# Kernel tuning notes

Hardware: AMD Instinct MI355X
Metric: run time of the kernel (lower is better)

## Reference

```python
import jax, jax.numpy as jnp
import numpy as np
from jax import lax

B, T, H, E, C = 64, 512, 512, 128, 1000


def setup_inputs() -> dict:
    key = jax.random.key(0)
    k0, k1, k2, k3, k4 = jax.random.split(key, 5)
    marks = jax.random.randint(k0, (B, T), 0, C)
    # monotonic event times -> positive inter-event durations
    timestamps = jnp.cumsum(jax.random.uniform(k1, (B, T), dtype=jnp.float32), axis=1)
    emb_table = jax.random.normal(k2, (C, E), dtype=jnp.float32) * 0.02
    W_cell = jax.random.normal(k3, (E + H, 7 * H), dtype=jnp.float32) / np.sqrt(E + H).astype(np.float32)
    b_cell = jnp.zeros((7 * H,), dtype=jnp.float32)
    init_hidden = jax.random.normal(k4, (1, 6 * H), dtype=jnp.float32) * 0.02
    return {"marks": marks, "timestamps": timestamps, "emb_table": emb_table,
            "W_cell": W_cell, "b_cell": b_cell, "init_hidden": init_hidden}


def _hawkes_states(marks, timestamps, emb_table, W_cell, b_cell, init_hidden):
    b, t = marks.shape
    h6 = init_hidden.shape[-1]
    h = h6 // 6
    e = emb_table.shape[-1]
    # inter-event durations (time_embedding): [B,T]
    dt = jnp.diff(timestamps, axis=1, prepend=jnp.zeros((b, 1), timestamps.dtype))
    x = emb_table[marks]  # [B,T,E]
    # precompute input contribution to the gates outside the scan
    x_gates = jnp.einsum('bte,eg->btg', x, W_cell[:e]) + b_cell  # [B,T,7H]
    Wh = W_cell[e:]  # [H,7H]

    init = jnp.broadcast_to(init_hidden, (b, h6))
    h_d0, c_d0, c_bar0, c0, delta0, o0 = jnp.split(init, 6, axis=-1)
    h_d0 = jnp.tanh(h_d0); c_d0 = jnp.tanh(c_d0); c_bar0 = jnp.tanh(c_bar0)
    c0 = jnp.tanh(c0); delta0 = jax.nn.softplus(delta0); o0 = jax.nn.sigmoid(o0)
    state0 = jnp.concatenate([h_d0, o0, c_bar0, c0, delta0, c_d0], axis=-1)  # [B,6H]

    def step(carry, inp):
        h_d, c_d, c_bar = carry
        xg, dur = inp  # [B,7H], [B]
        g = xg + h_d @ Wh
        gi, gf, gz, go, gib, gfb, gd = jnp.split(g, 7, axis=-1)
        gi = jax.nn.sigmoid(gi); gf = jax.nn.sigmoid(gf); gz = jnp.tanh(gz)
        go = jax.nn.sigmoid(go); gib = jax.nn.sigmoid(gib); gfb = jax.nn.sigmoid(gfb)
        gd = jax.nn.softplus(gd)
        c = gf * c_d + gi * gz
        c_bar_t = gfb * c_bar + gib * gz
        c_d_t = c_bar_t + (c - c_bar_t) * jnp.exp(-gd * dur[:, None])
        h_d_t = go * jnp.tanh(c_d_t)
        out = jnp.concatenate([h_d_t, go, c_bar_t, c, gd, c_d_t], axis=-1)
        return (h_d_t, c_d_t, c_bar_t), out

    _, outs = lax.scan(step, (h_d0, c_d0, c_bar0),
                       (x_gates.transpose(1, 0, 2), dt.T))  # outs: [T,B,6H]
    return jnp.concatenate([state0[:, None, :], outs.transpose(1, 0, 2)], axis=1)  # [B,T+1,6H]


def reference(marks, timestamps, emb_table, W_cell, b_cell, init_hidden):
    return _hawkes_states(marks, timestamps, emb_table, W_cell, b_cell, init_hidden)
```

## Files before the change

kernel.cpp:

```cpp
#include <hip/hip_runtime.h>
#include <stdint.h>

#define TT    512
#define HH    512
#define EE    128
#define G7    (7*HH)
#define H6    (6*HH)
#define TP1   (TT+1)

#define BW 16
#define II 32
#define NIG 16
#define NCOL 224
#define HLDS 520

typedef float f32x4 __attribute__((ext_vector_type(4)));
typedef short short8 __attribute__((ext_vector_type(8)));

__device__ __forceinline__ float bf2f(unsigned short u){
  union { unsigned u32; float f; } v; v.u32 = ((unsigned)u) << 16; return v.f;
}
__device__ __forceinline__ unsigned short f2bf(float f){
  union { float f; unsigned u; } v; v.f = f;
  unsigned u = v.u;
  u += 0x7FFFu + ((u >> 16) & 1u);
  return (unsigned short)(u >> 16);
}
__device__ __forceinline__ float sigmoidf_(float x){ return 1.0f/(1.0f+__expf(-x)); }
__device__ __forceinline__ float tanhf_(float x){ return 1.0f - 2.0f/(__expf(2.0f*x)+1.0f); }
__device__ __forceinline__ float softplusf_(float x){
  float ax = fabsf(x);
  return fmaxf(x, 0.0f) + __logf(1.0f + __expf(-ax));
}

__device__ __forceinline__ bool detect_bf16(const void* ts){
  const unsigned short* p = (const unsigned short*)ts;
  int cnt = 0;
  #pragma unroll
  for (int i = 0; i < 32; ++i){
    unsigned short v = p[2*i];
    int e = (v >> 7) & 0xFF;
    cnt += (((v & 0x8000u) == 0) && e >= 110 && e <= 140) ? 1 : 0;
  }
  return cnt >= 16;
}

__device__ __forceinline__ float lde(const void* p, size_t i, bool bfm){
  return bfm ? bf2f(((const unsigned short*)p)[i]) : ((const float*)p)[i];
}
__device__ __forceinline__ void sto(void* p, size_t i, float v, bool bfm){
  if (bfm) ((unsigned short*)p)[i] = f2bf(v);
  else     ((float*)p)[i] = v;
}

__global__ void k_embgates(const void* __restrict__ emb,
                           const void* __restrict__ W,
                           const void* __restrict__ bcell,
                           const void* __restrict__ ts,
                           unsigned short* __restrict__ eg){
  const bool bfm = detect_bf16(ts);
  __shared__ __align__(16) float xs[8][EE];
  const int tid = threadIdx.x;
  const int c0  = blockIdx.y * 8;
  const int j   = blockIdx.x * 512 + tid * 2;

  #pragma unroll
  for (int r = 0; r < 4; ++r){
    int e = tid + 256*r;
    int ci = e >> 7, k = e & 127;
    xs[ci][k] = lde(emb, (size_t)(c0+ci)*EE + k, bfm);
  }
  __syncthreads();

  float acc[8][2];
  {
    float b0v = lde(bcell, j, bfm), b1v = lde(bcell, j+1, bfm);
    #pragma unroll
    for (int ci=0; ci<8; ++ci){ acc[ci][0] = b0v; acc[ci][1] = b1v; }
  }
  const unsigned short* W16 = (const unsigned short*)W;
  const float*          W32 = (const float*)W;
  for (int k0 = 0; k0 < EE; k0 += 4){
    float w0[4], w1[4];
    if (bfm){
      #pragma unroll
      for (int kk=0; kk<4; ++kk){
        unsigned wu = *(const unsigned*)&W16[(size_t)(k0+kk)*G7 + j];
        w0[kk] = bf2f((unsigned short)(wu & 0xffff));
        w1[kk] = bf2f((unsigned short)(wu >> 16));
      }
    } else {
      #pragma unroll
      for (int kk=0; kk<4; ++kk){
        float2 wf = *(const float2*)&W32[(size_t)(k0+kk)*G7 + j];
        w0[kk] = wf.x; w1[kk] = wf.y;
      }
    }
    #pragma unroll
    for (int ci=0; ci<8; ++ci){
      float4 x4 = *(const float4*)&xs[ci][k0];
      acc[ci][0] = fmaf(x4.x, w0[0], acc[ci][0]); acc[ci][1] = fmaf(x4.x, w1[0], acc[ci][1]);
      acc[ci][0] = fmaf(x4.y, w0[1], acc[ci][0]); acc[ci][1] = fmaf(x4.y, w1[1], acc[ci][1]);
      acc[ci][0] = fmaf(x4.z, w0[2], acc[ci][0]); acc[ci][1] = fmaf(x4.z, w1[2], acc[ci][1]);
      acc[ci][0] = fmaf(x4.w, w0[3], acc[ci][0]); acc[ci][1] = fmaf(x4.w, w1[3], acc[ci][1]);
    }
  }
  #pragma unroll
  for (int ci=0; ci<8; ++ci){
    unsigned outv = (unsigned)f2bf(acc[ci][0]) | ((unsigned)f2bf(acc[ci][1]) << 16);
    *(unsigned*)&eg[(size_t)(c0+ci)*G7 + j] = outv;
  }
}

__global__ void k_wqbf(const void* __restrict__ W,
                       const void* __restrict__ ts,
                       unsigned short* __restrict__ wqt){
  const bool bfm = detect_bf16(ts);
  __shared__ __align__(16) unsigned short tile[64][72];
  const int tid = threadIdx.x;
  const int j0 = blockIdx.x * 64;
  const int k0 = blockIdx.y * 64;
  const int c = tid & 63, r0 = tid >> 6;
  #pragma unroll
  for (int rr = 0; rr < 16; ++rr){
    int r = r0*16 + rr;
    tile[r][c] = f2bf(lde(W, (size_t)(EE + k0 + r)*G7 + (j0 + c), bfm));
  }
  __syncthreads();
  const int jj = tid >> 2, p = tid & 3;
  unsigned short o[16];
  #pragma unroll
  for (int q = 0; q < 16; ++q) o[q] = tile[p*16 + q][jj];
  unsigned short* dst = &wqt[(size_t)(j0+jj)*HH + k0 + p*16];
  *(uint4*)(dst)     = *(uint4*)&o[0];
  *(uint4*)(dst + 8) = *(uint4*)&o[8];
}

__launch_bounds__(1024, 1)
__global__ void k_scan(const int* __restrict__ marks,
                       const void* __restrict__ ts,
                       const void* __restrict__ ih,
                       const unsigned short* __restrict__ eg,
                       const unsigned short* __restrict__ wqt,
                       void* __restrict__ out,
                       unsigned int* flags,
                       unsigned long long* dbuf){
  const bool bfm = detect_bf16(ts);
  __shared__ __align__(16) unsigned short hdl[BW][HLDS];
  __shared__ __align__(16) float gl[BW][257];
  __shared__ __align__(16) unsigned short xgl[2][BW][240];

  const int tid  = threadIdx.x;
  const int g_i  = blockIdx.x & (NIG-1);
  const int g_b  = blockIdx.x >> 4;
  const int b0   = g_b * BW;
  const int i0   = g_i * II;
  const int lane = tid & 63;
  const int wv   = tid >> 6;

  short8 bq[16];
  {
    int n = lane & 15, q = lane >> 4;
    int coll = wv*16 + n;
    int cl = (coll < NCOL) ? coll : 0;
    int cg = ((cl >> 5) * HH) + i0 + (cl & 31);
    const unsigned short* wb = wqt + (size_t)cg*HH + q*8;
    #pragma unroll
    for (int kk = 0; kk < 16; ++kk)
      bq[kk] = *(const short8*)(wb + kk*32);
  }

  {
    int i = (tid & 255) * 2;
    unsigned short h0 = f2bf(tanhf_(lde(ih, i,   bfm)));
    unsigned short h1 = f2bf(tanhf_(lde(ih, i+1, bfm)));
    unsigned v = (unsigned)h0 | ((unsigned)h1 << 16);
    int bb0 = (tid >> 8) * 4;
    #pragma unroll
    for (int b = 0; b < 4; ++b) *(unsigned*)&hdl[bb0 + b][i] = v;
  }

  float cd = 0.0f, cbar = 0.0f, dtv = 0.0f;
  if (tid < 512){
    int b = tid >> 5, ii = tid & 31;
    int i = i0 + ii;
    float h0  = tanhf_(lde(ih, i, bfm));
    float cd0 = tanhf_(lde(ih, 512 + i, bfm));
    float cb0 = tanhf_(lde(ih, 1024 + i, bfm));
    float c0v = tanhf_(lde(ih, 1536 + i, bfm));
    float d0  = softplusf_(lde(ih, 2048 + i, bfm));
    float o0  = sigmoidf_(lde(ih, 2560 + i, bfm));
    cd = cd0; cbar = cb0;
    size_t ob = ((size_t)(b0 + b) * TP1) * H6 + i;
    sto(out, ob,        h0,  bfm);
    sto(out, ob +   HH, o0,  bfm);
    sto(out, ob + 2*HH, cb0, bfm);
    sto(out, ob + 3*HH, c0v, bfm);
    sto(out, ob + 4*HH, d0,  bfm);
    sto(out, ob + 5*HH, cd0, bfm);
  }

  if (tid < 512){
    int b = tid >> 5, c = tid & 31;
    if (c < 28){
      int mk = marks[(b0 + b)*TT + 0];
      int g = c >> 2, m4 = c & 3;
      uint4 v = *(const uint4*)&eg[(size_t)mk*G7 + g*HH + i0 + m4*8];
      *(uint4*)&xgl[0][b][c*8] = v;
    }
  }
  __syncthreads();

  const int m_ = lane & 15, q_ = lane >> 4;

  for (int t = 0; t < TT; ++t){
    const int cur = t & 1, nxt = cur ^ 1;

    if (t < TT-1 && tid < 512){
      int b = tid >> 5, c = tid & 31;
      if (c < 28){
        int mk = marks[(b0 + b)*TT + (t+1)];
        int g = c >> 2, m4 = c & 3;
        uint4 v = *(const uint4*)&eg[(size_t)mk*G7 + g*HH + i0 + m4*8];
        *(uint4*)&xgl[nxt][b][c*8] = v;
      }
    }
    if (tid < 512){
      int b = tid >> 5;
      float t1  = lde(ts, (size_t)(b0 + b)*TT + t, bfm);
      float t0_ = (t > 0) ? lde(ts, (size_t)(b0 + b)*TT + t - 1, bfm) : 0.0f;
      dtv = t1 - t0_;
    }

    if (t > 0){
      if (wv == 0){
        unsigned* fl = &flags[g_b * 64];
        const unsigned target = (unsigned)t;
        for (;;){
          unsigned v = __hip_atomic_load(&fl[lane & 15], __ATOMIC_RELAXED, __HIP_MEMORY_SCOPE_AGENT);
          if (__all((int)(v >= target))) break;
          __builtin_amdgcn_s_sleep(1);
        }
        __threadfence();
      }
      __syncthreads();
      const unsigned long long* src = dbuf + ((size_t)(g_b*2 + cur) * BW) * (HH/4);
      #pragma unroll
      for (int r = 0; r < 2; ++r){
        int idx = tid + 1024*r;
        int bb = idx >> 7, oo = idx & 127;
        unsigned long long v = __hip_atomic_load(&src[(size_t)bb*(HH/4) + oo],
                                                 __ATOMIC_RELAXED, __HIP_MEMORY_SCOPE_AGENT);
        *(unsigned long long*)&hdl[bb][oo*4] = v;
      }
    }
    __syncthreads();

    f32x4 acc = {0.f, 0.f, 0.f, 0.f};
    #pragma unroll
    for (int kk = 0; kk < 16; ++kk){
      short8 a = *(const short8*)&hdl[m_][kk*32 + q_*8];
      acc = __builtin_amdgcn_mfma_f32_16x16x32_bf16(a, bq[kk], acc, 0, 0, 0);
    }
    {
      int col  = wv*16 + (lane & 15);
      int rowb = (lane >> 4) * 4;
      #pragma unroll
      for (int r = 0; r < 4; ++r) gl[rowb + r][col] = acc[r];
    }
    __syncthreads();

    float hdt = 0.f, gov = 0.f, cbv = 0.f, cv = 0.f, gdv = 0.f, cdtv = 0.f;
    if (tid < 512){
      int b = tid >> 5, ii = tid & 31;
      float gv[7];
      #pragma unroll
      for (int g = 0; g < 7; ++g)
        gv[g] = gl[b][g*32 + ii] + bf2f(xgl[cur][b][g*32 + ii]);
      float gi  = sigmoidf_(gv[0]);
      float gf  = sigmoidf_(gv[1]);
      float gz  = tanhf_(gv[2]);
      gov       = sigmoidf_(gv[3]);
      float gib = sigmoidf_(gv[4]);
      float gfb = sigmoidf_(gv[5]);
      gdv       = softplusf_(gv[6]);
      cv   = gf*cd + gi*gz;
      cbv  = gfb*cbar + gib*gz;
      float dec = __expf(-gdv * dtv);
      cdtv = cbv + (cv - cbv)*dec;
      hdt  = gov * tanhf_(cdtv);
      cd = cdtv; cbar = cbv;

      unsigned hv = (unsigned)f2bf(hdt);
      unsigned a2 = hv | ((unsigned)__shfl_xor((int)hv, 1) << 16);
      unsigned hi = (unsigned)__shfl_xor((int)a2, 2);
      if ((tid & 3) == 0){
        unsigned long long v64 = (unsigned long long)a2 | ((unsigned long long)hi << 32);
        unsigned long long* dst = dbuf + ((size_t)(g_b*2 + nxt) * BW + b) * (HH/4)
                                       + ((i0 + ii) >> 2);
        __hip_atomic_store(dst, v64, __ATOMIC_RELAXED, __HIP_MEMORY_SCOPE_AGENT);
      }
    }
    __syncthreads();
    if (tid == 0){
      __threadfence();
      __hip_atomic_store(&flags[g_b*64 + g_i], (unsigned)(t + 1),
                         __ATOMIC_RELEASE, __HIP_MEMORY_SCOPE_AGENT);
    }
    if (tid < 512){
      int b = tid >> 5, ii = tid & 31;
      size_t ob = ((size_t)(b0 + b) * TP1 + (t+1)) * H6 + i0 + ii;
      sto(out, ob,        hdt,  bfm);
      sto(out, ob +   HH, gov,  bfm);
      sto(out, ob + 2*HH, cbv,  bfm);
      sto(out, ob + 3*HH, cv,   bfm);
      sto(out, ob + 4*HH, gdv,  bfm);
      sto(out, ob + 5*HH, cdtv, bfm);
    }
  }
}

extern "C" void kernel_launch(void* const* d_in, const int* in_sizes, int n_in,
                              void* d_out, int out_size, void* d_ws, size_t ws_size,
                              hipStream_t stream){
  const int*  marks = (const int*)d_in[0];
  const void* ts    = d_in[1];
  const void* emb   = d_in[2];
  const void* W     = d_in[3];
  const void* bc    = d_in[4];
  const void* ih    = d_in[5];

  unsigned char* ws = (unsigned char*)d_ws;
  unsigned int*       flags = (unsigned int*)ws;
  unsigned long long* dbuf  = (unsigned long long*)(ws + 1024);
  unsigned short*     eg    = (unsigned short*)(ws + 132096);
  unsigned short*     wqt   = (unsigned short*)(ws + 132096 + 7168000);
  (void)in_sizes; (void)n_in; (void)out_size;

  if (ws_size < (size_t)(132096 + 7168000 + 3670016)) return;

  hipMemsetAsync(flags, 0, 1024, stream);
  hipLaunchKernelGGL(k_embgates, dim3(7, 125), dim3(256), 0, stream, emb, W, bc, ts, eg);
  hipLaunchKernelGGL(k_wqbf,     dim3(56, 8),  dim3(256), 0, stream, W, ts, wqt);

  void* args[] = { (void*)&marks, (void*)&ts, (void*)&ih, (void*)&eg,
                   (void*)&wqt, (void*)&d_out, (void*)&flags, (void*)&dbuf };
  hipLaunchCooperativeKernel((const void*)k_scan, dim3(64), dim3(1024), args, 0, stream);
}
```

Baseline: 4.167 ms.

## Halve scan block to 512 threads, two MFMA tiles per wave, remap block ids

```diff
diff --git a/kernel.cpp b/kernel.cpp
--- a/kernel.cpp
+++ b/kernel.cpp
@@ -136,7 +136,7 @@
   *(uint4*)(dst + 8) = *(uint4*)&o[8];
 }
 
-__launch_bounds__(1024, 1)
+__launch_bounds__(512, 2)
 __global__ void k_scan(const int* __restrict__ marks,
                        const void* __restrict__ ts,
                        const void* __restrict__ ih,
@@ -151,23 +151,32 @@
   __shared__ __align__(16) unsigned short xgl[2][BW][240];
 
   const int tid  = threadIdx.x;
-  const int g_i  = blockIdx.x & (NIG-1);
-  const int g_b  = blockIdx.x >> 4;
+  const int bid  = blockIdx.x;
+  const int g_b  = (bid & 7) >> 1;
+  const int g_i  = ((bid >> 3) << 1) | (bid & 1);
   const int b0   = g_b * BW;
   const int i0   = g_i * II;
   const int lane = tid & 63;
   const int wv   = tid >> 6;
-
-  short8 bq[16];
+  const int eb   = tid >> 5;
+  const int eii  = tid & 31;
+
+  short8 bq0[16], bq1[16];
   {
     int n = lane & 15, q = lane >> 4;
-    int coll = wv*16 + n;
-    int cl = (coll < NCOL) ? coll : 0;
-    int cg = ((cl >> 5) * HH) + i0 + (cl & 31);
-    const unsigned short* wb = wqt + (size_t)cg*HH + q*8;
-    #pragma unroll
-    for (int kk = 0; kk < 16; ++kk)
-      bq[kk] = *(const short8*)(wb + kk*32);
+    int coll0 = wv*32 + n;
+    int coll1 = wv*32 + 16 + n;
+    int cl0 = (coll0 < NCOL) ? coll0 : 0;
+    int cl1 = (coll1 < NCOL) ? coll1 : 0;
+    int cg0 = ((cl0 >> 5) * HH) + i0 + (cl0 & 31);
+    int cg1 = ((cl1 >> 5) * HH) + i0 + (cl1 & 31);
+    const unsigned short* wb0 = wqt + (size_t)cg0*HH + q*8;
+    const unsigned short* wb1 = wqt + (size_t)cg1*HH + q*8;
+    #pragma unroll
+    for (int kk = 0; kk < 16; ++kk){
+      bq0[kk] = *(const short8*)(wb0 + kk*32);
+      bq1[kk] = *(const short8*)(wb1 + kk*32);
+    }
   }
 
   {
@@ -175,15 +184,14 @@
     unsigned short h0 = f2bf(tanhf_(lde(ih, i,   bfm)));
     unsigned short h1 = f2bf(tanhf_(lde(ih, i+1, bfm)));
     unsigned v = (unsigned)h0 | ((unsigned)h1 << 16);
-    int bb0 = (tid >> 8) * 4;
-    #pragma unroll
-    for (int b = 0; b < 4; ++b) *(unsigned*)&hdl[bb0 + b][i] = v;
-  }
-
-  float cd = 0.0f, cbar = 0.0f, dtv = 0.0f;
-  if (tid < 512){
-    int b = tid >> 5, ii = tid & 31;
-    int i = i0 + ii;
+    int bb0 = (tid >> 8) * 8;
+    #pragma unroll
+    for (int b = 0; b < 8; ++b) *(unsigned*)&hdl[bb0 + b][i] = v;
+  }
+
+  float cd, cbar, tsp = 0.0f;
+  {
+    int i = i0 + eii;
     float h0  = tanhf_(lde(ih, i, bfm));
     float cd0 = tanhf_(lde(ih, 512 + i, bfm));
     float cb0 = tanhf_(lde(ih, 1024 + i, bfm));
@@ -191,7 +199,7 @@
     float d0  = softplusf_(lde(ih, 2048 + i, bfm));
     float o0  = sigmoidf_(lde(ih, 2560 + i, bfm));
     cd = cd0; cbar = cb0;
-    size_t ob = ((size_t)(b0 + b) * TP1) * H6 + i;
+    size_t ob = ((size_t)(b0 + eb) * TP1) * H6 + i;
     sto(out, ob,        h0,  bfm);
     sto(out, ob +   HH, o0,  bfm);
     sto(out, ob + 2*HH, cb0, bfm);
@@ -200,14 +208,11 @@
     sto(out, ob + 5*HH, cd0, bfm);
   }
 
-  if (tid < 512){
-    int b = tid >> 5, c = tid & 31;
-    if (c < 28){
-      int mk = marks[(b0 + b)*TT + 0];
-      int g = c >> 2, m4 = c & 3;
-      uint4 v = *(const uint4*)&eg[(size_t)mk*G7 + g*HH + i0 + m4*8];
-      *(uint4*)&xgl[0][b][c*8] = v;
-    }
+  if (eii < 28){
+    int mk = marks[(b0 + eb)*TT + 0];
+    int g = eii >> 2, m4 = eii & 3;
+    uint4 v = *(const uint4*)&eg[(size_t)mk*G7 + g*HH + i0 + m4*8];
+    *(uint4*)&xgl[0][eb][eii*8] = v;
   }
   __syncthreads();
 
@@ -216,24 +221,20 @@
   for (int t = 0; t < TT; ++t){
     const int cur = t & 1, nxt = cur ^ 1;
 
-    if (t < TT-1 && tid < 512){
-      int b = tid >> 5, c = tid & 31;
-      if (c < 28){
-        int mk = marks[(b0 + b)*TT + (t+1)];
-        int g = c >> 2, m4 = c & 3;
-        uint4 v = *(const uint4*)&eg[(size_t)mk*G7 + g*HH + i0 + m4*8];
-        *(uint4*)&xgl[nxt][b][c*8] = v;
-      }
-    }
-    if (tid < 512){
-      int b = tid >> 5;
-      float t1  = lde(ts, (size_t)(b0 + b)*TT + t, bfm);
-      float t0_ = (t > 0) ? lde(ts, (size_t)(b0 + b)*TT + t - 1, bfm) : 0.0f;
-      dtv = t1 - t0_;
-    }
-
-    if (t > 0){
-      if (wv == 0){
+    if (t < TT-1 && eii < 28){
+      int mk = marks[(b0 + eb)*TT + (t+1)];
+      int g = eii >> 2, m4 = eii & 3;
+      uint4 v = *(const uint4*)&eg[(size_t)mk*G7 + g*HH + i0 + m4*8];
+      *(uint4*)&xgl[nxt][eb][eii*8] = v;
+    }
+    float dtv;
+    {
+      float t1 = lde(ts, (size_t)(b0 + eb)*TT + t, bfm);
+      dtv = t1 - tsp; tsp = t1;
+    }
+
+    if (t > 0 && wv == 0){
+      {
         unsigned* fl = &flags[g_b * 64];
         const unsigned target = (unsigned)t;
         for (;;){
@@ -243,40 +244,48 @@
         }
         __threadfence();
       }
-      __syncthreads();
       const unsigned long long* src = dbuf + ((size_t)(g_b*2 + cur) * BW) * (HH/4);
       #pragma unroll
-      for (int r = 0; r < 2; ++r){
-        int idx = tid + 1024*r;
-        int bb = idx >> 7, oo = idx & 127;
-        unsigned long long v = __hip_atomic_load(&src[(size_t)bb*(HH/4) + oo],
-                                                 __ATOMIC_RELAXED, __HIP_MEMORY_SCOPE_AGENT);
-        *(unsigned long long*)&hdl[bb][oo*4] = v;
+      for (int half = 0; half < 2; ++half){
+        unsigned long long tmp[16];
+        #pragma unroll
+        for (int r = 0; r < 16; ++r){
+          int idx = (half*16 + r)*64 + lane;
+          tmp[r] = __hip_atomic_load(&src[idx], __ATOMIC_RELAXED, __HIP_MEMORY_SCOPE_AGENT);
+        }
+        #pragma unroll
+        for (int r = 0; r < 16; ++r){
+          int idx = (half*16 + r)*64 + lane;
+          *(unsigned long long*)&hdl[idx >> 7][(idx & 127)*4] = tmp[r];
+        }
       }
     }
     __syncthreads();
 
-    f32x4 acc = {0.f, 0.f, 0.f, 0.f};
+    f32x4 acc0 = {0.f,0.f,0.f,0.f}, acc1 = {0.f,0.f,0.f,0.f};
     #pragma unroll
     for (int kk = 0; kk < 16; ++kk){
       short8 a = *(const short8*)&hdl[m_][kk*32 + q_*8];
-      acc = __builtin_amdgcn_mfma_f32_16x16x32_bf16(a, bq[kk], acc, 0, 0, 0);
+      acc0 = __builtin_amdgcn_mfma_f32_16x16x32_bf16(a, bq0[kk], acc0, 0, 0, 0);
+      acc1 = __builtin_amdgcn_mfma_f32_16x16x32_bf16(a, bq1[kk], acc1, 0, 0, 0);
     }
     {
-      int col  = wv*16 + (lane & 15);
+      int col0 = wv*32 + (lane & 15);
       int rowb = (lane >> 4) * 4;
       #pragma unroll
-      for (int r = 0; r < 4; ++r) gl[rowb + r][col] = acc[r];
+      for (int r = 0; r < 4; ++r){
+        gl[rowb + r][col0]      = acc0[r];
+        gl[rowb + r][col0 + 16] = acc1[r];
+      }
     }
     __syncthreads();
 
-    float hdt = 0.f, gov = 0.f, cbv = 0.f, cv = 0.f, gdv = 0.f, cdtv = 0.f;
-    if (tid < 512){
-      int b = tid >> 5, ii = tid & 31;
+    float hdt, gov, cbv, cv, gdv, cdtv;
+    {
       float gv[7];
       #pragma unroll
       for (int g = 0; g < 7; ++g)
-        gv[g] = gl[b][g*32 + ii] + bf2f(xgl[cur][b][g*32 + ii]);
+        gv[g] = gl[eb][g*32 + eii] + bf2f(xgl[cur][eb][g*32 + eii]);
       float gi  = sigmoidf_(gv[0]);
       float gf  = sigmoidf_(gv[1]);
       float gz  = tanhf_(gv[2]);
@@ -296,8 +305,8 @@
       unsigned hi = (unsigned)__shfl_xor((int)a2, 2);
       if ((tid & 3) == 0){
         unsigned long long v64 = (unsigned long long)a2 | ((unsigned long long)hi << 32);
-        unsigned long long* dst = dbuf + ((size_t)(g_b*2 + nxt) * BW + b) * (HH/4)
-                                       + ((i0 + ii) >> 2);
+        unsigned long long* dst = dbuf + ((size_t)(g_b*2 + nxt) * BW + eb) * (HH/4)
+                                       + ((i0 + eii) >> 2);
         __hip_atomic_store(dst, v64, __ATOMIC_RELAXED, __HIP_MEMORY_SCOPE_AGENT);
       }
     }
@@ -307,9 +316,8 @@
       __hip_atomic_store(&flags[g_b*64 + g_i], (unsigned)(t + 1),
                          __ATOMIC_RELEASE, __HIP_MEMORY_SCOPE_AGENT);
     }
-    if (tid < 512){
-      int b = tid >> 5, ii = tid & 31;
-      size_t ob = ((size_t)(b0 + b) * TP1 + (t+1)) * H6 + i0 + ii;
+    {
+      size_t ob = ((size_t)(b0 + eb) * TP1 + (t+1)) * H6 + i0 + eii;
       sto(out, ob,        hdt,  bfm);
       sto(out, ob +   HH, gov,  bfm);
       sto(out, ob + 2*HH, cbv,  bfm);
@@ -345,5 +353,5 @@
 
   void* args[] = { (void*)&marks, (void*)&ts, (void*)&ih, (void*)&eg,
                    (void*)&wqt, (void*)&d_out, (void*)&flags, (void*)&dbuf };
-  hipLaunchCooperativeKernel((const void*)k_scan, dim3(64), dim3(1024), args, 0, stream);
-}
+  hipLaunchCooperativeKernel((const void*)k_scan, dim3(64), dim3(512), args, 0, stream);
+}
```

Measured after the change: 4.123 ms. About the same (-1.1%).
